# Performance work log

Hardware: AMD Instinct MI355X
Metric: run time of the kernel (lower is better)

Reference implementation:

```python
import jax, jax.numpy as jnp
import numpy as np

THRESHOLD = 0.5
NEG_POS_RATIO = 3
ALPHA = 1.0
B, P, C, O = 64, 8732, 81, 32


def setup_inputs() -> dict:
    key = jax.random.key(0)
    k1, k2, k3, k4, k5, k6 = jax.random.split(key, 6)
    pred_locs = jax.random.normal(k1, (B, P, 4), dtype=jnp.float32)
    pred_scores = jax.random.normal(k2, (B, P, C), dtype=jnp.float32)
    # valid ground-truth corner boxes: sample center/size, convert to xy, clip to [0,1]
    ctr = jax.random.uniform(k3, (B, O, 2), minval=0.1, maxval=0.9)
    wh = jax.random.uniform(k4, (B, O, 2), minval=0.05, maxval=0.4)
    boxes = jnp.clip(jnp.concatenate([ctr - wh / 2, ctr + wh / 2], axis=-1), 0.0, 1.0)
    labels = jax.random.randint(k5, (B, O), 1, C, dtype=jnp.int64)
    pc = jax.random.uniform(k6, (P, 2), minval=0.05, maxval=0.95)
    pwh = jax.random.uniform(jax.random.fold_in(k6, 1), (P, 2), minval=0.05, maxval=0.3)
    priors_cxcy = jnp.concatenate([pc, pwh], axis=-1)
    return {"pred_locs": pred_locs, "pred_scores": pred_scores,
            "boxes": boxes, "labels": labels, "priors_cxcy": priors_cxcy}


def _jaccard(b, priors_xy):
    # b: [O,4] xy, priors_xy: [P,4] xy -> [O,P]
    lo = jnp.maximum(b[:, None, :2], priors_xy[None, :, :2])
    hi = jnp.minimum(b[:, None, 2:], priors_xy[None, :, 2:])
    inter = jnp.prod(jnp.clip(hi - lo, 0.0), axis=-1)
    area_b = jnp.prod(b[:, 2:] - b[:, :2], axis=-1)
    area_p = jnp.prod(priors_xy[:, 2:] - priors_xy[:, :2], axis=-1)
    return inter / (area_b[:, None] + area_p[None, :] - inter)


def _forward(pred_locs, pred_scores, boxes, labels, priors_cxcy):
    priors_xy = jnp.concatenate([priors_cxcy[:, :2] - priors_cxcy[:, 2:] / 2,
                                 priors_cxcy[:, :2] + priors_cxcy[:, 2:] / 2], axis=1)
    n_obj = boxes.shape[1]

    def match(b, l):
        ov = _jaccard(b, priors_xy)                      # [O,P]
        ov_fp = jnp.max(ov, axis=0)                      # [P]
        obj_fp = jnp.argmax(ov, axis=0)                  # [P]
        prior_fo = jnp.argmax(ov, axis=1)                # [O]
        obj_fp = obj_fp.at[prior_fo].set(jnp.arange(n_obj))
        ov_fp = ov_fp.at[prior_fo].set(1.0)
        lab = jnp.where(ov_fp < THRESHOLD, 0, l[obj_fp]) # [P]
        pt = b[obj_fp]                                   # [P,4] xy
        c = jnp.concatenate([(pt[:, 2:] + pt[:, :2]) / 2, pt[:, 2:] - pt[:, :2]], axis=1)
        g = jnp.concatenate([(c[:, :2] - priors_cxcy[:, :2]) / (priors_cxcy[:, 2:] / 10),
                             jnp.log(c[:, 2:] / priors_cxcy[:, 2:]) * 5], axis=1)
        return g, lab

    true_locs, true_classes = jax.vmap(match)(boxes, labels)  # [B,P,4], [B,P]

    pos = true_classes != 0                                   # [B,P]
    n_pos = jnp.sum(pos, axis=1)                              # [B]
    n_pos_total = jnp.sum(n_pos).astype(pred_locs.dtype)

    # L1Loss (mean over positive elements, 4 coords each)
    loc_abs = jnp.abs(pred_locs - true_locs) * pos[..., None].astype(pred_locs.dtype)
    loc_loss = jnp.sum(loc_abs) / (n_pos_total * 4.0)

    # per-prior cross entropy
    logp = jax.nn.log_softmax(pred_scores, axis=-1)           # [B,P,C]
    ce = -jnp.take_along_axis(logp, true_classes[..., None], axis=-1)[..., 0]  # [B,P]

    posf = pos.astype(ce.dtype)
    conf_pos_sum = jnp.sum(ce * posf)
    conf_neg = jnp.where(pos, 0.0, ce)
    conf_neg_sorted = -jnp.sort(-conf_neg, axis=1)            # descending
    ranks = jnp.arange(ce.shape[1])[None, :]
    hard = ranks < (NEG_POS_RATIO * n_pos)[:, None]
    conf_hard_neg_sum = jnp.sum(conf_neg_sorted * hard.astype(ce.dtype))

    conf_loss = (conf_hard_neg_sum + conf_pos_sum) / n_pos_total
    return conf_loss + ALPHA * loc_loss


def reference(pred_locs, pred_scores, boxes, labels, priors_cxcy):
    return _forward(pred_locs, pred_scores, boxes, labels, priors_cxcy)
```

## Files before the change

kernel.cpp:

```cpp
#include <hip/hip_runtime.h>

#define BB 64
#define PP 8732
#define OO 32
#define CC 81
#define NEGPOS 3
#define NSL_A 18
#define NCH_B 32
#define CHB 273
#define NCH_CE 69

#define WS_POVFP  0
#define WS_BESTP  (WS_POVFP + BB*PP*8)
#define WS_CENEG  (WS_BESTP + BB*NCH_B*OO*8)
#define WS_CEPOS  (WS_CENEG + BB*PP*4)
#define WS_LSUMB  (WS_CEPOS + BB*NCH_CE*4)
#define WS_NPOSB  (WS_LSUMB + BB*NCH_CE*4)
#define WS_HARDB  (WS_NPOSB + BB*NCH_CE*4)
#define WS_DONE   (WS_HARDB + BB*4)

__global__ __launch_bounds__(512) void match_geom(
    const float* __restrict__ boxes, const float* __restrict__ priors,
    unsigned long long* __restrict__ povfp, unsigned long long* __restrict__ bestp,
    int* __restrict__ done)
{
    const int b = blockIdx.y, gx = blockIdx.x, tid = threadIdx.x;
    __shared__ float sbx[OO * 4];
    __shared__ unsigned long long sred[8 * OO];
    if (tid < OO * 4) sbx[tid] = boxes[b * OO * 4 + tid];
    if (gx == 0 && b == 0 && tid == 0) *done = 0;
    __syncthreads();

    if (gx < NSL_A) {
        const int p = gx * 512 + tid;
        if (p >= PP) return;
        float4 pr = ((const float4*)priors)[p];
        float plx = pr.x - pr.z * 0.5f, ply = pr.y - pr.w * 0.5f;
        float phx = pr.x + pr.z * 0.5f, phy = pr.y + pr.w * 0.5f;
        float parea = pr.z * pr.w;
        float bestv = -1.0f; int besto = 0;
#pragma unroll
        for (int o = 0; o < OO; ++o) {
            float b0 = sbx[o*4+0], b1 = sbx[o*4+1], b2 = sbx[o*4+2], b3 = sbx[o*4+3];
            float lox = fmaxf(b0, plx), loy = fmaxf(b1, ply);
            float hix = fminf(b2, phx), hiy = fminf(b3, phy);
            float inter = fmaxf(hix - lox, 0.0f) * fmaxf(hiy - loy, 0.0f);
            float iou = inter / ((b2 - b0) * (b3 - b1) + parea - inter);
            if (iou > bestv) { bestv = iou; besto = o; }
        }
        povfp[b * PP + p] = ((unsigned long long)__float_as_uint(bestv) << 32) | (unsigned)besto;
    } else {
        const int ch = gx - NSL_A;
        const int o = tid & 31, sub = tid >> 5;
        const float b0 = sbx[o*4+0], b1 = sbx[o*4+1], b2 = sbx[o*4+2], b3 = sbx[o*4+3];
        const float barea = (b2 - b0) * (b3 - b1);
        const int base = ch * CHB;
        unsigned long long best = 0ull;
        for (int i = sub; i < CHB; i += 16) {
            int p = base + i;
            if (p >= PP) break;
            float4 pr = ((const float4*)priors)[p];
            float plx = pr.x - pr.z * 0.5f, ply = pr.y - pr.w * 0.5f;
            float phx = pr.x + pr.z * 0.5f, phy = pr.y + pr.w * 0.5f;
            float parea = pr.z * pr.w;
            float lox = fmaxf(b0, plx), loy = fmaxf(b1, ply);
            float hix = fminf(b2, phx), hiy = fminf(b3, phy);
            float inter = fmaxf(hix - lox, 0.0f) * fmaxf(hiy - loy, 0.0f);
            float iou = inter / (barea + parea - inter);
            unsigned long long enc =
                ((unsigned long long)__float_as_uint(iou) << 32) | (unsigned)(~(unsigned)p);
            best = (enc > best) ? enc : best;
        }
        unsigned long long w = __shfl_down(best, 32, 64);
        best = (w > best) ? w : best;
        const int wid = tid >> 6, lane = tid & 63;
        if (lane < 32) sred[wid * OO + o] = best;
        __syncthreads();
        if (tid < OO) {
            unsigned long long m = 0ull;
#pragma unroll
            for (int wv = 0; wv < 8; ++wv) {
                unsigned long long v = sred[wv * OO + tid];
                m = (v > m) ? v : m;
            }
            bestp[(b * NCH_B + ch) * OO + tid] = m;
        }
    }
}

__global__ __launch_bounds__(128) void ce_match(
    const float* __restrict__ scores, const float* __restrict__ pred_locs,
    const float* __restrict__ boxes, const int* __restrict__ labels,
    const float* __restrict__ priors,
    const unsigned long long* __restrict__ povfp,
    const unsigned long long* __restrict__ bestp,
    float* __restrict__ ce_neg, float* __restrict__ cepos,
    float* __restrict__ lsum_bc, int* __restrict__ npos_bc)
{
    __shared__ float ss[128 * CC];
    __shared__ float sbx[OO * 4];
    __shared__ int   slab[OO];
    __shared__ int   spfo[OO];
    __shared__ signed char sovr[128];
    __shared__ float srf[2], srl[2];
    __shared__ int   sri[2];

    const int b = blockIdx.y, ch = blockIdx.x, tid = threadIdx.x;
    const int base = ch * 128;
    const int nval = (PP - base < 128) ? (PP - base) : 128;

    const float4* __restrict__ src =
        (const float4*)(scores + ((long long)b * PP + base) * CC);
    float4* dst = (float4*)ss;
    const int n4 = (nval * CC) / 4;
    for (int i = tid; i < n4; i += 128) dst[i] = src[i];

    if (tid < OO * 4) sbx[tid] = boxes[b * OO * 4 + tid];
    if (tid < OO)     slab[tid] = labels[b * OO + tid];
    if (tid < OO) {
        unsigned long long m = 0ull;
        for (int c = 0; c < NCH_B; ++c) {
            unsigned long long v = bestp[(b * NCH_B + c) * OO + tid];
            m = (v > m) ? v : m;
        }
        spfo[tid] = (int)(~(unsigned)(m & 0xFFFFFFFFull));
    }
    sovr[tid] = -1;
    __syncthreads();
    if (tid == 0) {
        for (int o = 0; o < OO; ++o) {
            int p = spfo[o] - base;
            if (p >= 0 && p < 128) sovr[p] = (signed char)o;
        }
    }
    __syncthreads();

    float pos = 0.0f, lsum = 0.0f; int lpos = 0;
    if (tid < nval) {
        const int p = base + tid;
        const float* v = ss + tid * CC;
        float m = v[0];
#pragma unroll
        for (int c = 1; c < CC; ++c) m = fmaxf(m, v[c]);
        float sum = 0.0f;
#pragma unroll
        for (int c = 0; c < CC; ++c) sum += __expf(v[c] - m);
        float lse = m + __logf(sum);

        unsigned long long pv = povfp[b * PP + p];
        int o = (int)(pv & 0xFFu);
        float ov = __uint_as_float((unsigned)(pv >> 32));
        int ovr = sovr[tid];
        if (ovr >= 0) { o = ovr; ov = 1.0f; }
        int l = (ov < 0.5f) ? 0 : slab[o];
        float ce = lse - v[l];
        ce_neg[b * PP + p] = (l != 0) ? 0.0f : ce;
        if (l != 0) {
            pos = ce; lpos = 1;
            float b0 = sbx[o*4+0], b1 = sbx[o*4+1], b2 = sbx[o*4+2], b3 = sbx[o*4+3];
            float4 pr = ((const float4*)priors)[p];
            float gx = ((b0 + b2) * 0.5f - pr.x) / (pr.z * 0.1f);
            float gy = ((b1 + b3) * 0.5f - pr.y) / (pr.w * 0.1f);
            float gw = logf((b2 - b0) / pr.z) * 5.0f;
            float gh = logf((b3 - b1) / pr.w) * 5.0f;
            float4 pl = ((const float4*)pred_locs)[b * PP + p];
            lsum = fabsf(pl.x - gx) + fabsf(pl.y - gy) + fabsf(pl.z - gw) + fabsf(pl.w - gh);
        }
    }
    for (int off = 32; off > 0; off >>= 1) {
        pos  += __shfl_down(pos, off, 64);
        lsum += __shfl_down(lsum, off, 64);
        lpos += __shfl_down(lpos, off, 64);
    }
    if ((tid & 63) == 0) { int w = tid >> 6; srf[w] = pos; srl[w] = lsum; sri[w] = lpos; }
    __syncthreads();
    if (tid == 0) {
        cepos[b * NCH_CE + ch]   = srf[0] + srf[1];
        lsum_bc[b * NCH_CE + ch] = srl[0] + srl[1];
        npos_bc[b * NCH_CE + ch] = sri[0] + sri[1];
    }
}

__global__ __launch_bounds__(512) void topk_kernel(
    const float* __restrict__ ce_neg, const int* __restrict__ npos_bc,
    const float* __restrict__ cepos, const float* __restrict__ lsum_bc,
    float* __restrict__ hard_b, int* __restrict__ done, float* __restrict__ out)
{
    __shared__ float sv[PP];
    __shared__ int hist[256 * 16];
    __shared__ int ssum[256];
    __shared__ unsigned sel[2];
    __shared__ float sr[8];
    __shared__ int sK;
    const int b = blockIdx.x, tid = threadIdx.x;
    for (int p = tid; p < PP; p += 512) sv[p] = ce_neg[b * PP + p];
    if (tid == 0) {
        int n = 0;
        for (int c = 0; c < NCH_CE; ++c) n += npos_bc[b * NCH_CE + c];
        int k = NEGPOS * n;
        sK = (k > PP) ? PP : k;
    }
    __syncthreads();
    const int K = sK;

    float hard = 0.0f;
    if (K > 0) {
        unsigned prefix = 0, mask = 0;
        unsigned remaining = (unsigned)K;
        for (int pass = 0; pass < 4; ++pass) {
            const int shift = 24 - 8 * pass;
            for (int i = tid; i < 256 * 16; i += 512) hist[i] = 0;
            __syncthreads();
            for (int p = tid; p < PP; p += 512) {
                unsigned u = __float_as_uint(sv[p]);
                if ((u & mask) == prefix)
                    atomicAdd(&hist[(((u >> shift) & 255) << 4) | (tid & 15)], 1);
            }
            __syncthreads();
            if (tid < 256) {
                int s = 0;
#pragma unroll
                for (int w = 0; w < 16; ++w) s += hist[(tid << 4) | w];
                ssum[tid] = s;
            }
            __syncthreads();
            for (int off = 1; off < 256; off <<= 1) {
                int v = 0;
                if (tid < 256) v = (tid + off < 256) ? ssum[tid + off] : 0;
                __syncthreads();
                if (tid < 256) ssum[tid] += v;
                __syncthreads();
            }
            if (tid < 256 && (unsigned)ssum[tid] >= remaining &&
                (tid == 255 || (unsigned)ssum[tid + 1] < remaining)) {
                sel[0] = (unsigned)tid;
                sel[1] = remaining - ((tid == 255) ? 0u : (unsigned)ssum[tid + 1]);
            }
            __syncthreads();
            prefix |= sel[0] << shift;
            mask |= 0xFFu << shift;
            remaining = sel[1];
            __syncthreads();
        }
        float sgt = 0.0f;
        for (int p = tid; p < PP; p += 512) {
            unsigned u = __float_as_uint(sv[p]);
            if (u > prefix) sgt += sv[p];
        }
        for (int off = 32; off > 0; off >>= 1) sgt += __shfl_down(sgt, off, 64);
        if ((tid & 63) == 0) sr[tid >> 6] = sgt;
        __syncthreads();
        if (tid == 0) {
            hard = 0.0f;
#pragma unroll
            for (int w = 0; w < 8; ++w) hard += sr[w];
            hard += __uint_as_float(prefix) * (float)remaining;
        }
    }
    __shared__ int sticket;
    if (tid == 0) {
        hard_b[b] = hard;
        __threadfence();
        sticket = atomicAdd(done, 1);
    }
    __syncthreads();
    if (sticket != BB - 1) return;

    float cpos = 0.0f, labs = 0.0f, chard = 0.0f; int n = 0;
    for (int i = tid; i < BB * NCH_CE; i += 512) {
        cpos += cepos[i];
        labs += lsum_bc[i];
        n    += npos_bc[i];
    }
    if (tid < BB) chard = atomicAdd(&hard_b[tid], 0.0f);
    for (int off = 32; off > 0; off >>= 1) {
        cpos  += __shfl_down(cpos, off, 64);
        labs  += __shfl_down(labs, off, 64);
        chard += __shfl_down(chard, off, 64);
        n     += __shfl_down(n, off, 64);
    }
    __shared__ float f0[8], f1[8], f2[8];
    __shared__ int i3[8];
    if ((tid & 63) == 0) { int w = tid >> 6; f0[w] = cpos; f1[w] = labs; f2[w] = chard; i3[w] = n; }
    __syncthreads();
    if (tid == 0) {
        float a = 0.0f, bs = 0.0f, c = 0.0f; int nt = 0;
#pragma unroll
        for (int w = 0; w < 8; ++w) { a += f0[w]; bs += f1[w]; c += f2[w]; nt += i3[w]; }
        float nf = (float)nt;
        out[0] = (c + a) / nf + bs / (nf * 4.0f);
    }
}

extern "C" void kernel_launch(void* const* d_in, const int* in_sizes, int n_in,
                              void* d_out, int out_size, void* d_ws, size_t ws_size,
                              hipStream_t stream) {
    const float* pred_locs   = (const float*)d_in[0];
    const float* pred_scores = (const float*)d_in[1];
    const float* boxes       = (const float*)d_in[2];
    const int*   labels      = (const int*)d_in[3];
    const float* priors      = (const float*)d_in[4];
    float* out = (float*)d_out;

    char* ws = (char*)d_ws;
    unsigned long long* povfp = (unsigned long long*)(ws + WS_POVFP);
    unsigned long long* bestp = (unsigned long long*)(ws + WS_BESTP);
    float* ce_neg  = (float*)(ws + WS_CENEG);
    float* cepos   = (float*)(ws + WS_CEPOS);
    float* lsum_bc = (float*)(ws + WS_LSUMB);
    int*   nposbc  = (int*)(ws + WS_NPOSB);
    float* hard_b  = (float*)(ws + WS_HARDB);
    int*   done    = (int*)(ws + WS_DONE);

    match_geom<<<dim3(NSL_A + NCH_B, BB), 512, 0, stream>>>(boxes, priors, povfp, bestp, done);
    ce_match<<<dim3(NCH_CE, BB), 128, 0, stream>>>(pred_scores, pred_locs, boxes, labels,
                                                   priors, povfp, bestp,
                                                   ce_neg, cepos, lsum_bc, nposbc);
    topk_kernel<<<BB, 512, 0, stream>>>(ce_neg, nposbc, cepos, lsum_bc, hard_b, done, out);
}
```

Baseline: 364.7 us.

## Split CE from matching and compute log-softmax with four threads per prior

Splits the combined CE-and-match kernel into a label-assignment kernel and a dedicated cross-entropy kernel. The new CE kernel assigns four lanes per prior, reads scores straight from global memory, and reduces max and sum with shuffles. This replaces the 41 KB shared-memory staging that limited occupancy in the old kernel. The match output is also split into separate float and byte arrays to cut traffic. The cost is an extra kernel launch and a workspace round-trip for the labels.

```diff
diff --git a/kernel.cpp b/kernel.cpp
--- a/kernel.cpp
+++ b/kernel.cpp
@@ -8,21 +8,25 @@
 #define NSL_A 18
 #define NCH_B 32
 #define CHB 273
-#define NCH_CE 69
-
-#define WS_POVFP  0
-#define WS_BESTP  (WS_POVFP + BB*PP*8)
-#define WS_CENEG  (WS_BESTP + BB*NCH_B*OO*8)
+#define NSL_C 8
+#define SLC 1092
+#define NCE 8732
+
+#define WS_POVF   0
+#define WS_POVO   (WS_POVF  + BB*PP*4)
+#define WS_BESTP  (WS_POVO  + BB*PP)
+#define WS_LAB    (WS_BESTP + BB*NCH_B*OO*8)
+#define WS_CENEG  (WS_LAB   + BB*PP)
 #define WS_CEPOS  (WS_CENEG + BB*PP*4)
-#define WS_LSUMB  (WS_CEPOS + BB*NCH_CE*4)
-#define WS_NPOSB  (WS_LSUMB + BB*NCH_CE*4)
-#define WS_HARDB  (WS_NPOSB + BB*NCH_CE*4)
+#define WS_LSUMB  (WS_CEPOS + NCE*4)
+#define WS_NPOSB  (WS_LSUMB + BB*NSL_C*4)
+#define WS_HARDB  (WS_NPOSB + BB*NSL_C*4)
 #define WS_DONE   (WS_HARDB + BB*4)
 
 __global__ __launch_bounds__(512) void match_geom(
     const float* __restrict__ boxes, const float* __restrict__ priors,
-    unsigned long long* __restrict__ povfp, unsigned long long* __restrict__ bestp,
-    int* __restrict__ done)
+    float* __restrict__ povf, unsigned char* __restrict__ povo,
+    unsigned long long* __restrict__ bestp, int* __restrict__ done)
 {
     const int b = blockIdx.y, gx = blockIdx.x, tid = threadIdx.x;
     __shared__ float sbx[OO * 4];
@@ -48,7 +52,8 @@
             float iou = inter / ((b2 - b0) * (b3 - b1) + parea - inter);
             if (iou > bestv) { bestv = iou; besto = o; }
         }
-        povfp[b * PP + p] = ((unsigned long long)__float_as_uint(bestv) << 32) | (unsigned)besto;
+        povf[b * PP + p] = bestv;
+        povo[b * PP + p] = (unsigned char)besto;
     } else {
         const int ch = gx - NSL_A;
         const int o = tid & 31, sub = tid >> 5;
@@ -88,32 +93,22 @@
     }
 }
 
-__global__ __launch_bounds__(128) void ce_match(
-    const float* __restrict__ scores, const float* __restrict__ pred_locs,
-    const float* __restrict__ boxes, const int* __restrict__ labels,
-    const float* __restrict__ priors,
-    const unsigned long long* __restrict__ povfp,
+__global__ __launch_bounds__(256) void match_b(
+    const float* __restrict__ pred_locs, const float* __restrict__ boxes,
+    const int* __restrict__ labels, const float* __restrict__ priors,
+    const float* __restrict__ povf, const unsigned char* __restrict__ povo,
     const unsigned long long* __restrict__ bestp,
-    float* __restrict__ ce_neg, float* __restrict__ cepos,
-    float* __restrict__ lsum_bc, int* __restrict__ npos_bc)
+    signed char* __restrict__ lab_out, int* __restrict__ npos_bs,
+    float* __restrict__ lsum_bs)
 {
-    __shared__ float ss[128 * CC];
+    const int b = blockIdx.y, sl = blockIdx.x, tid = threadIdx.x;
+    const int base = sl * SLC;
     __shared__ float sbx[OO * 4];
     __shared__ int   slab[OO];
     __shared__ int   spfo[OO];
-    __shared__ signed char sovr[128];
-    __shared__ float srf[2], srl[2];
-    __shared__ int   sri[2];
-
-    const int b = blockIdx.y, ch = blockIdx.x, tid = threadIdx.x;
-    const int base = ch * 128;
-    const int nval = (PP - base < 128) ? (PP - base) : 128;
-
-    const float4* __restrict__ src =
-        (const float4*)(scores + ((long long)b * PP + base) * CC);
-    float4* dst = (float4*)ss;
-    const int n4 = (nval * CC) / 4;
-    for (int i = tid; i < n4; i += 128) dst[i] = src[i];
+    __shared__ signed char sovr[SLC];
+    __shared__ float sredf[4];
+    __shared__ int   sredi[4];
 
     if (tid < OO * 4) sbx[tid] = boxes[b * OO * 4 + tid];
     if (tid < OO)     slab[tid] = labels[b * OO + tid];
@@ -125,38 +120,28 @@
         }
         spfo[tid] = (int)(~(unsigned)(m & 0xFFFFFFFFull));
     }
-    sovr[tid] = -1;
+    for (int i = tid; i < SLC; i += 256) sovr[i] = -1;
     __syncthreads();
     if (tid == 0) {
         for (int o = 0; o < OO; ++o) {
             int p = spfo[o] - base;
-            if (p >= 0 && p < 128) sovr[p] = (signed char)o;
-        }
-    }
-    __syncthreads();
-
-    float pos = 0.0f, lsum = 0.0f; int lpos = 0;
-    if (tid < nval) {
-        const int p = base + tid;
-        const float* v = ss + tid * CC;
-        float m = v[0];
-#pragma unroll
-        for (int c = 1; c < CC; ++c) m = fmaxf(m, v[c]);
-        float sum = 0.0f;
-#pragma unroll
-        for (int c = 0; c < CC; ++c) sum += __expf(v[c] - m);
-        float lse = m + __logf(sum);
-
-        unsigned long long pv = povfp[b * PP + p];
-        int o = (int)(pv & 0xFFu);
-        float ov = __uint_as_float((unsigned)(pv >> 32));
-        int ovr = sovr[tid];
+            if (p >= 0 && p < SLC) sovr[p] = (signed char)o;
+        }
+    }
+    __syncthreads();
+
+    float lsum = 0.0f; int lpos = 0;
+    for (int i = tid; i < SLC; i += 256) {
+        int p = base + i;
+        if (p >= PP) break;
+        int o = (int)povo[b * PP + p];
+        float ov = povf[b * PP + p];
+        int ovr = sovr[i];
         if (ovr >= 0) { o = ovr; ov = 1.0f; }
         int l = (ov < 0.5f) ? 0 : slab[o];
-        float ce = lse - v[l];
-        ce_neg[b * PP + p] = (l != 0) ? 0.0f : ce;
+        lab_out[b * PP + p] = (signed char)l;
         if (l != 0) {
-            pos = ce; lpos = 1;
+            lpos++;
             float b0 = sbx[o*4+0], b1 = sbx[o*4+1], b2 = sbx[o*4+2], b3 = sbx[o*4+3];
             float4 pr = ((const float4*)priors)[p];
             float gx = ((b0 + b2) * 0.5f - pr.x) / (pr.z * 0.1f);
@@ -164,26 +149,74 @@
             float gw = logf((b2 - b0) / pr.z) * 5.0f;
             float gh = logf((b3 - b1) / pr.w) * 5.0f;
             float4 pl = ((const float4*)pred_locs)[b * PP + p];
-            lsum = fabsf(pl.x - gx) + fabsf(pl.y - gy) + fabsf(pl.z - gw) + fabsf(pl.w - gh);
+            lsum += fabsf(pl.x - gx) + fabsf(pl.y - gy) + fabsf(pl.z - gw) + fabsf(pl.w - gh);
         }
     }
     for (int off = 32; off > 0; off >>= 1) {
-        pos  += __shfl_down(pos, off, 64);
         lsum += __shfl_down(lsum, off, 64);
         lpos += __shfl_down(lpos, off, 64);
     }
-    if ((tid & 63) == 0) { int w = tid >> 6; srf[w] = pos; srl[w] = lsum; sri[w] = lpos; }
-    __syncthreads();
-    if (tid == 0) {
-        cepos[b * NCH_CE + ch]   = srf[0] + srf[1];
-        lsum_bc[b * NCH_CE + ch] = srl[0] + srl[1];
-        npos_bc[b * NCH_CE + ch] = sri[0] + sri[1];
-    }
+    if ((tid & 63) == 0) { sredf[tid >> 6] = lsum; sredi[tid >> 6] = lpos; }
+    __syncthreads();
+    if (tid == 0) {
+        float s = 0.0f; int n = 0;
+#pragma unroll
+        for (int w = 0; w < 4; ++w) { s += sredf[w]; n += sredi[w]; }
+        lsum_bs[b * NSL_C + sl] = s;
+        npos_bs[b * NSL_C + sl] = n;
+    }
+}
+
+__global__ __launch_bounds__(256) void ce_kernel(
+    const float* __restrict__ scores, const signed char* __restrict__ lab,
+    float* __restrict__ ce_neg, float* __restrict__ cepos)
+{
+    const int tid = threadIdx.x;
+    const int g = tid >> 2, j = tid & 3;
+    const int bp = blockIdx.x * 64 + g;
+    const float* __restrict__ v = scores + (long long)bp * CC;
+    const int l = (int)lab[bp];
+
+    float d[21];
+#pragma unroll
+    for (int k = 0; k < 5; ++k) {
+        const int c4 = (4 * k + j) * 4;
+#pragma unroll
+        for (int q = 0; q < 4; ++q) d[4*k+q] = v[c4 + q];
+    }
+    d[20] = (j == 0) ? v[80] : -3.0e38f;
+
+    float m = d[20];
+#pragma unroll
+    for (int i = 0; i < 20; ++i) m = fmaxf(m, d[i]);
+    m = fmaxf(m, __shfl_xor(m, 1, 64));
+    m = fmaxf(m, __shfl_xor(m, 2, 64));
+
+    float s = 0.0f;
+#pragma unroll
+    for (int i = 0; i < 21; ++i) s += __expf(d[i] - m);
+
+    float vl = 0.0f;
+    if (l == 80) { if (j == 0) vl = d[20]; }
+    else { int c = l >> 2; if ((c & 3) == j) vl = d[4 * (c >> 2) + (l & 3)]; }
+
+    s  += __shfl_xor(s, 1, 64);   s  += __shfl_xor(s, 2, 64);
+    vl += __shfl_xor(vl, 1, 64);  vl += __shfl_xor(vl, 2, 64);
+
+    float ce = m + __logf(s) - vl;
+    if (j == 0) ce_neg[bp] = (l != 0) ? 0.0f : ce;
+    float posc = (l != 0 && j == 0) ? ce : 0.0f;
+
+    for (int off = 32; off > 0; off >>= 1) posc += __shfl_down(posc, off, 64);
+    __shared__ float sr[4];
+    if ((tid & 63) == 0) sr[tid >> 6] = posc;
+    __syncthreads();
+    if (tid == 0) cepos[blockIdx.x] = sr[0] + sr[1] + sr[2] + sr[3];
 }
 
 __global__ __launch_bounds__(512) void topk_kernel(
-    const float* __restrict__ ce_neg, const int* __restrict__ npos_bc,
-    const float* __restrict__ cepos, const float* __restrict__ lsum_bc,
+    const float* __restrict__ ce_neg, const int* __restrict__ npos_bs,
+    const float* __restrict__ cepos, const float* __restrict__ lsum_bs,
     float* __restrict__ hard_b, int* __restrict__ done, float* __restrict__ out)
 {
     __shared__ float sv[PP];
@@ -196,7 +229,7 @@
     for (int p = tid; p < PP; p += 512) sv[p] = ce_neg[b * PP + p];
     if (tid == 0) {
         int n = 0;
-        for (int c = 0; c < NCH_CE; ++c) n += npos_bc[b * NCH_CE + c];
+        for (int c = 0; c < NSL_C; ++c) n += npos_bs[b * NSL_C + c];
         int k = NEGPOS * n;
         sK = (k > PP) ? PP : k;
     }
@@ -225,10 +258,10 @@
             }
             __syncthreads();
             for (int off = 1; off < 256; off <<= 1) {
-                int v = 0;
-                if (tid < 256) v = (tid + off < 256) ? ssum[tid + off] : 0;
+                int vv = 0;
+                if (tid < 256) vv = (tid + off < 256) ? ssum[tid + off] : 0;
                 __syncthreads();
-                if (tid < 256) ssum[tid] += v;
+                if (tid < 256) ssum[tid] += vv;
                 __syncthreads();
             }
             if (tid < 256 && (unsigned)ssum[tid] >= remaining &&
@@ -267,11 +300,8 @@
     if (sticket != BB - 1) return;
 
     float cpos = 0.0f, labs = 0.0f, chard = 0.0f; int n = 0;
-    for (int i = tid; i < BB * NCH_CE; i += 512) {
-        cpos += cepos[i];
-        labs += lsum_bc[i];
-        n    += npos_bc[i];
-    }
+    for (int i = tid; i < NCE; i += 512) cpos += cepos[i];
+    for (int i = tid; i < BB * NSL_C; i += 512) { labs += lsum_bs[i]; n += npos_bs[i]; }
     if (tid < BB) chard = atomicAdd(&hard_b[tid], 0.0f);
     for (int off = 32; off > 0; off >>= 1) {
         cpos  += __shfl_down(cpos, off, 64);
@@ -303,18 +333,20 @@
     float* out = (float*)d_out;
 
     char* ws = (char*)d_ws;
-    unsigned long long* povfp = (unsigned long long*)(ws + WS_POVFP);
+    float* povf = (float*)(ws + WS_POVF);
+    unsigned char* povo = (unsigned char*)(ws + WS_POVO);
     unsigned long long* bestp = (unsigned long long*)(ws + WS_BESTP);
+    signed char* lab = (signed char*)(ws + WS_LAB);
     float* ce_neg  = (float*)(ws + WS_CENEG);
     float* cepos   = (float*)(ws + WS_CEPOS);
-    float* lsum_bc = (float*)(ws + WS_LSUMB);
-    int*   nposbc  = (int*)(ws + WS_NPOSB);
+    float* lsum_bs = (float*)(ws + WS_LSUMB);
+    int*   nposbs  = (int*)(ws + WS_NPOSB);
     float* hard_b  = (float*)(ws + WS_HARDB);
     int*   done    = (int*)(ws + WS_DONE);
 
-    match_geom<<<dim3(NSL_A + NCH_B, BB), 512, 0, stream>>>(boxes, priors, povfp, bestp, done);
-    ce_match<<<dim3(NCH_CE, BB), 128, 0, stream>>>(pred_scores, pred_locs, boxes, labels,
-                                                   priors, povfp, bestp,
-                                                   ce_neg, cepos, lsum_bc, nposbc);
-    topk_kernel<<<BB, 512, 0, stream>>>(ce_neg, nposbc, cepos, lsum_bc, hard_b, done, out);
-}
+    match_geom<<<dim3(NSL_A + NCH_B, BB), 512, 0, stream>>>(boxes, priors, povf, povo, bestp, done);
+    match_b<<<dim3(NSL_C, BB), 256, 0, stream>>>(pred_locs, boxes, labels, priors,
+                                                 povf, povo, bestp, lab, nposbs, lsum_bs);
+    ce_kernel<<<NCE, 256, 0, stream>>>(pred_scores, lab, ce_neg, cepos);
+    topk_kernel<<<BB, 512, 0, stream>>>(ce_neg, nposbs, cepos, lsum_bs, hard_b, done, out);
+}
```

Result: faster. 321.4 us (-11.9%).
